# Kernel tuning notes

Hardware: AMD Instinct MI355X
Metric: run time of the kernel (lower is better)

The kernel has to match this reference:

```python
import jax, jax.numpy as jnp
import numpy as np

TEMPERATURE = 0.07
UNIFORMITY_THRESHOLD = 0.1
SEPARATION_MARGIN = 2.0
W_SUPCON = 1.0
W_SEPARATION = 0.5
W_UNIFORMITY = 0.5
NUM_MASKS = 6


def setup_inputs() -> dict:
    key = jax.random.key(0)
    k1, k2, k3 = jax.random.split(key, 3)
    B, H, Wd, D = 16, 33, 33, 512
    emb = jax.random.normal(k1, (B, H, Wd, D), dtype=jnp.float32)
    emb = emb / jnp.linalg.norm(emb, axis=-1, keepdims=True)  # module expects normalized embeddings
    masks = jax.random.uniform(k2, (B, NUM_MASKS, H, Wd), dtype=jnp.float32)
    is_forged = jax.random.uniform(k3, (B,), dtype=jnp.float32)
    return {"embeddings": emb, "masks": masks, "is_forged": is_forged}


def _labels(masks):
    # masks: (M, H, W). Channel i writes label i+1 where mask>0.5 (if channel has any mass);
    # later channels overwrite earlier -> equivalent to max over active hits.
    active = masks.sum(axis=(1, 2)) > 0  # (M,)
    hit = (masks > 0.5) & active[:, None, None]
    ids = jnp.arange(1, masks.shape[0] + 1)[:, None, None]
    return jnp.max(jnp.where(hit, ids, 0), axis=0).reshape(-1)  # (H*W,)


def _per_image(emb, masks, forged):
    H, W, D = emb.shape
    feat = emb.reshape(-1, D)  # (N, D)
    N = feat.shape[0]
    labels = _labels(masks)  # (N,) in 0..M
    L = masks.shape[0] + 1  # possible labels 0..6
    onehot = (labels[:, None] == jnp.arange(L)[None, :]).astype(feat.dtype)  # (N, L)
    cnt = onehot.sum(axis=0)  # (L,)
    sums = onehot.T @ feat  # (L, D) per-label sums
    mean_l = sums / jnp.maximum(cnt, 1.0)[:, None]  # safe per-label centroids

    # ---- SupCon (PixelSupConLoss) ----
    logits = (feat @ feat.T) / TEMPERATURE  # (N, N)
    logits = logits - jax.lax.stop_gradient(logits.max(axis=1, keepdims=True))
    same = (labels[:, None] == labels[None, :]).astype(feat.dtype)
    logits_mask = 1.0 - jnp.eye(N, dtype=feat.dtype)
    pos = same * logits_mask
    exp_l = jnp.exp(logits) * logits_mask
    log_prob = logits - jnp.log(exp_l.sum(axis=1, keepdims=True) + 1e-6)
    pos_sum = pos.sum(axis=1)
    mean_lp = (pos * log_prob).sum(axis=1) / jnp.where(pos_sum == 0, 1.0, pos_sum)
    anchor_valid = (pos_sum > 0).astype(feat.dtype)
    n_anchor = anchor_valid.sum()
    supcon = (-mean_lp * anchor_valid).sum() / jnp.maximum(n_anchor, 1.0)
    supcon_valid = n_anchor > 0

    # ---- Inter-instance separation ----
    present = cnt > 0
    cn = (mean_l ** 2).sum(axis=1)  # (L,)
    sq = cn[:, None] + cn[None, :] - 2.0 * (mean_l @ mean_l.T)  # squared centroid dists
    tri = jnp.triu(jnp.ones((L, L), dtype=bool), k=1)
    pair_valid = tri & present[:, None] & present[None, :]
    d = jnp.sqrt(jnp.where(pair_valid, jnp.maximum(sq, 0.0), 1.0))
    terms = jnp.where(pair_valid, jax.nn.relu(SEPARATION_MARGIN - d), 0.0)
    n_pairs = pair_valid.sum().astype(feat.dtype)
    sep = terms.sum() / jnp.maximum(n_pairs, 1.0)
    sep_valid = present.sum() >= 2

    # ---- Uniformity ----
    rn2 = (feat ** 2).sum(axis=1)  # (N,)
    q_l = onehot.T @ rn2  # (L,) per-label sum of squared norms
    var_l = q_l / jnp.maximum(cnt, 1.0) - (mean_l ** 2).sum(axis=1)  # E||e||^2 - ||mean||^2
    lbl_valid = (cnt >= 2) & (var_l > UNIFORMITY_THRESHOLD)
    inst_loss = jnp.where(lbl_valid, var_l - UNIFORMITY_THRESHOLD, 0.0).sum()
    n_lbl = lbl_valid.sum().astype(feat.dtype)
    uni_forged = inst_loss / jnp.maximum(n_lbl, 1.0)
    uni_forged_valid = n_lbl > 0
    mean_all = feat.mean(axis=0)
    var_all = ((feat - mean_all) ** 2).sum(axis=1).mean()
    uni_unf = jnp.where(var_all > UNIFORMITY_THRESHOLD, var_all - UNIFORMITY_THRESHOLD, 0.0)
    uni_unf_valid = var_all > UNIFORMITY_THRESHOLD

    is_f = forged >= 0.5
    uni = jnp.where(is_f, uni_forged, uni_unf)
    uni_valid = jnp.where(is_f, uni_forged_valid, uni_unf_valid)
    return supcon, supcon_valid, sep, sep_valid, uni, uni_valid


def _agg(vals, valids):
    v = valids.astype(vals.dtype)
    n = v.sum()
    return jnp.where(n > 0, (vals * v).sum() / jnp.maximum(n, 1.0), 0.0)


def reference(embeddings, masks, is_forged):
    sc, scv, sp, spv, un, unv = jax.vmap(_per_image)(embeddings, masks, is_forged)
    supcon = _agg(sc, scv)
    separation = _agg(sp, spv)
    uniformity = _agg(un, unv)
    return W_SUPCON * supcon + W_SEPARATION * separation + W_UNIFORMITY * uniformity
```

## Files before the change

kernel.cpp:

```cpp
#include <hip/hip_runtime.h>
#include <math.h>

#define NPIX 1089
#define DIM 512
#define NIMG 16
#define NLBL 8
#define NMASK 6
#define INVT 14.2857142857142857f

#define NGRP 72
#define NROWPAD 1152
#define NT9 9


typedef short v8s __attribute__((ext_vector_type(8)));
typedef float v4f __attribute__((ext_vector_type(4)));

__device__ __forceinline__ float wave_reduce(float x) {
#pragma unroll
  for (int o = 32; o > 0; o >>= 1) x += __shfl_xor(x, o, 64);
  return x;
}
__device__ __forceinline__ unsigned bfbits(float x) {
  unsigned u = __float_as_uint(x);
  return (u + 0x7FFFu + ((u >> 16) & 1u)) >> 16;
}
__device__ __forceinline__ unsigned pk(float lo, float hi) {
  return bfbits(lo) | (bfbits(hi) << 16);
}

__global__ __launch_bounds__(512) void k_packsum(const float* __restrict__ emb,
                                                 const float* __restrict__ masks,
                                                 uint2* __restrict__ bfemb2,
                                                 float* __restrict__ sums9,
                                                 int* __restrict__ labels,
                                                 float* __restrict__ cnt9,
                                                 unsigned* __restrict__ counter) {
  int b = blockIdx.y;
  int g9 = blockIdx.x >> 1, dh = blockIdx.x & 1;
  int tid = threadIdx.x, dd = tid & 63, w4 = tid >> 6, lane = tid & 63;
  __shared__ float msum[NMASK];
  __shared__ int slab[128];
  __shared__ int scnt[NLBL];
  __shared__ float4 red[8 * 8 * 64];
  if (tid < NMASK) msum[tid] = 0.f;
  if (tid < NLBL) scnt[tid] = 0;
  if (b == 0 && blockIdx.x == 0 && tid == 0) *counter = 0u;
  __syncthreads();
  {
    float am[NMASK] = {0.f, 0.f, 0.f, 0.f, 0.f, 0.f};
    for (int p = tid; p < NPIX; p += 512) {
#pragma unroll
      for (int c = 0; c < NMASK; c++) am[c] += masks[((size_t)b * NMASK + c) * NPIX + p];
    }
#pragma unroll
    for (int c = 0; c < NMASK; c++) {
      float v = wave_reduce(am[c]);
      if (lane == 0) atomicAdd(&msum[c], v);
    }
  }
  __syncthreads();
  if (tid < 128) {
    int r = g9 * 128 + tid;
    int lab = 7;
    if (r < NPIX) {
      lab = 0;
#pragma unroll
      for (int c = 0; c < NMASK; c++) {
        float mv = masks[((size_t)b * NMASK + c) * NPIX + r];
        if (mv > 0.5f && msum[c] > 0.f) lab = c + 1;
      }
    }
    slab[tid] = lab;
    if (dh == 0) {
      labels[b * NROWPAD + r] = lab;
      if (r < NPIX) atomicAdd(&scnt[lab], 1);
    }
  }
  __syncthreads();
  if (dh == 0 && tid < NLBL) cnt9[((size_t)b * NT9 + g9) * NLBL + tid] = (float)scnt[tid];
  float4 fa0 = {0,0,0,0}, fa1 = {0,0,0,0}, fa2 = {0,0,0,0}, fa3 = {0,0,0,0};
  float4 fa4 = {0,0,0,0}, fa5 = {0,0,0,0}, fa6 = {0,0,0,0}, fa7 = {0,0,0,0};
  int kc = dh * 8 + (dd >> 3), q = (dd >> 1) & 3, half = dd & 1;
#pragma unroll
  for (int k = 0; k < 16; k++) {
    int r = g9 * 128 + w4 + k * 8;
    bool v = r < NPIX;
    int rc = v ? r : (NPIX - 1);
    float4 x = ((const float4*)(emb + (size_t)(b * NPIX + rc) * DIM))[dh * 64 + dd];
    if (!v) x = make_float4(0.f, 0.f, 0.f, 0.f);
    uint2 o = make_uint2(pk(x.x, x.y), pk(x.z, x.w));
    bfemb2[((((size_t)(b * NGRP + (r >> 4)) * 16 + kc) * 64) + q * 16 + (r & 15)) * 2 + half] = o;
    int lab = __builtin_amdgcn_readfirstlane(slab[r - g9 * 128]);
    switch (lab) {
      case 0: fa0.x += x.x; fa0.y += x.y; fa0.z += x.z; fa0.w += x.w; break;
      case 1: fa1.x += x.x; fa1.y += x.y; fa1.z += x.z; fa1.w += x.w; break;
      case 2: fa2.x += x.x; fa2.y += x.y; fa2.z += x.z; fa2.w += x.w; break;
      case 3: fa3.x += x.x; fa3.y += x.y; fa3.z += x.z; fa3.w += x.w; break;
      case 4: fa4.x += x.x; fa4.y += x.y; fa4.z += x.z; fa4.w += x.w; break;
      case 5: fa5.x += x.x; fa5.y += x.y; fa5.z += x.z; fa5.w += x.w; break;
      case 6: fa6.x += x.x; fa6.y += x.y; fa6.z += x.z; fa6.w += x.w; break;
      default: fa7.x += x.x; fa7.y += x.y; fa7.z += x.z; fa7.w += x.w; break;
    }
  }
  red[(0 * 8 + w4) * 64 + dd] = fa0; red[(1 * 8 + w4) * 64 + dd] = fa1;
  red[(2 * 8 + w4) * 64 + dd] = fa2; red[(3 * 8 + w4) * 64 + dd] = fa3;
  red[(4 * 8 + w4) * 64 + dd] = fa4; red[(5 * 8 + w4) * 64 + dd] = fa5;
  red[(6 * 8 + w4) * 64 + dd] = fa6; red[(7 * 8 + w4) * 64 + dd] = fa7;
  __syncthreads();
  int l = tid >> 6, d2 = tid & 63;
  float4 s = {0,0,0,0};
#pragma unroll
  for (int ww = 0; ww < 8; ww++) {
    float4 t = red[(l * 8 + ww) * 64 + d2];
    s.x += t.x; s.y += t.y; s.z += t.z; s.w += t.w;
  }
  *(float4*)&sums9[(((size_t)(b * NT9 + g9) * NLBL + l) * DIM) + dh * 256 + d2 * 4] = s;
}

__global__ __launch_bounds__(512) void k_epass5(const uint4* __restrict__ bfemb4,
                                                float* __restrict__ E9) {
  int n = blockIdx.x;
  int img = ((n & 7) << 1) | ((n >> 3) & 1);
  int t = n >> 4;
  int it = 0, rem = t;
  while (rem >= NT9 - it) { rem -= NT9 - it; it++; }
  int jt = it + rem;
  int i0 = it * 128, j0 = jt * 128;
  bool diag = (it == jt);
  int tid = threadIdx.x, lane = tid & 63, w = tid >> 6;
  int wm = w >> 2, wn = w & 3;
  int quad = lane >> 4, l15 = lane & 15;
  __shared__ float Ered[4][128];
  __shared__ float Ecol[2][128];

  size_t uA[4], uB[2];
#pragma unroll
  for (int f = 0; f < 4; f++)
    uA[f] = ((size_t)(img * NGRP + it * 8 + wm * 4 + f) * 16) * 64 + lane;
#pragma unroll
  for (int f = 0; f < 2; f++)
    uB[f] = ((size_t)(img * NGRP + jt * 8 + wn * 2 + f) * 16) * 64 + lane;

  v4f acc[4][2];
#pragma unroll
  for (int mf = 0; mf < 4; mf++)
#pragma unroll
    for (int nf = 0; nf < 2; nf++) acc[mf][nf] = (v4f){0.f, 0.f, 0.f, 0.f};

  v8s a0[4], b0[2], a1[4], b1[2];
#define LOADG(kc, AR, BR)                                               \
  {                                                                     \
    _Pragma("unroll") for (int f = 0; f < 4; f++)                       \
        AR[f] = *(const v8s*)(bfemb4 + uA[f] + (kc) * 64);              \
    _Pragma("unroll") for (int f = 0; f < 2; f++)                       \
        BR[f] = *(const v8s*)(bfemb4 + uB[f] + (kc) * 64);              \
  }
#define MFMAG(AR, BR)                                                   \
  {                                                                     \
    _Pragma("unroll") for (int mf = 0; mf < 4; mf++)                    \
        _Pragma("unroll") for (int nf = 0; nf < 2; nf++)                \
            acc[mf][nf] = __builtin_amdgcn_mfma_f32_16x16x32_bf16(      \
                AR[mf], BR[nf], acc[mf][nf], 0, 0, 0);                  \
  }

  LOADG(0, a0, b0);
#pragma unroll
  for (int kc = 0; kc < 16; kc += 2) {
    if (kc + 1 < 16) LOADG(kc + 1, a1, b1);
    MFMAG(a0, b0);
    if (kc + 2 < 16) LOADG(kc + 2, a0, b0);
    MFMAG(a1, b1);
  }
#undef LOADG
#undef MFMAG

  float scol[2] = {0.f, 0.f};
#pragma unroll
  for (int mf = 0; mf < 4; mf++) {
#pragma unroll
    for (int rr = 0; rr < 4; rr++) {
      int i = i0 + wm * 64 + mf * 16 + quad * 4 + rr;
      float srow = 0.f;
#pragma unroll
      for (int nf = 0; nf < 2; nf++) {
        int j = j0 + wn * 32 + nf * 16 + l15;
        float e = __expf((acc[mf][nf][rr] - 1.f) * INVT);
        bool ok = (j < NPIX) && (!diag || (i != j && i < NPIX));
        e = ok ? e : 0.f;
        srow += e;
        scol[nf] += e;
      }
      srow += __shfl_xor(srow, 1); srow += __shfl_xor(srow, 2);
      srow += __shfl_xor(srow, 4); srow += __shfl_xor(srow, 8);
      if (l15 == 0) Ered[wn][wm * 64 + mf * 16 + quad * 4 + rr] = srow;
    }
  }
  if (!diag) {
#pragma unroll
    for (int nf = 0; nf < 2; nf++) {
      float s = scol[nf];
      s += __shfl_xor(s, 16); s += __shfl_xor(s, 32);
      if (quad == 0) Ecol[wm][wn * 32 + nf * 16 + l15] = s;
    }
  }
  __syncthreads();
  if (tid < 128) {
    E9[((size_t)img * NT9 + jt) * NROWPAD + i0 + tid] =
        Ered[0][tid] + Ered[1][tid] + Ered[2][tid] + Ered[3][tid];
    if (!diag)
      E9[((size_t)img * NT9 + it) * NROWPAD + j0 + tid] = Ecol[0][tid] + Ecol[1][tid];
  }
}

__global__ __launch_bounds__(512) void k_imgfinal(const float* __restrict__ sums9,
                                                  const int* __restrict__ labels,
                                                  const float* __restrict__ cnt9,
                                                  const float* __restrict__ E9,
                                                  const float* __restrict__ is_forged,
                                                  unsigned* __restrict__ counter,
                                                  float* __restrict__ per_img,
                                                  float* __restrict__ out) {
  int b = blockIdx.x, tid = threadIdx.x;
  int wave = tid >> 6, lane = tid & 63;
  __shared__ float ssum[NLBL * DIM];
  __shared__ float sCnt[NLBL], sR[NLBL][NLBL];
  __shared__ float sLog, sNA;
  if (tid < NLBL) {
    float s = 0.f;
#pragma unroll
    for (int g = 0; g < NT9; g++) s += cnt9[((size_t)b * NT9 + g) * NLBL + tid];
    sCnt[tid] = s;
  }
  if (tid == 0) { sLog = 0.f; sNA = 0.f; }
  for (int o = tid; o < NLBL * DIM; o += 512) {
    float s = 0.f;
#pragma unroll
    for (int g = 0; g < NT9; g++) s += sums9[((size_t)(b * NT9 + g) * NLBL * DIM) + o];
    ssum[o] = s;
  }
  __syncthreads();
  float ll = 0.f, na = 0.f;
  for (int p = tid; p < NPIX; p += 512) {
    int lab = labels[b * NROWPAD + p];
    if (sCnt[lab] >= 1.5f) {
      float e = 0.f;
#pragma unroll
      for (int s = 0; s < NT9; s++) e += E9[((size_t)b * NT9 + s) * NROWPAD + p];
      ll += __logf(e + 1e-6f);
      na += 1.f;
    }
  }
  ll = wave_reduce(ll); na = wave_reduce(na);
  if (lane == 0) { atomicAdd(&sLog, ll); atomicAdd(&sNA, na); }
  for (int t = wave; t < 36; t += 8) {
    int a = 0, tt = t;
    while (tt >= NLBL - a) { tt -= NLBL - a; a++; }
    int bb = a + tt;
    float d0 = 0.f;
    for (int k = lane; k < DIM; k += 64) d0 += ssum[a * DIM + k] * ssum[bb * DIM + k];
    d0 = wave_reduce(d0);
    if (lane == 0) sR[a][bb] = d0;
  }
  __syncthreads();
  if (tid == 0) {
    float spos = 0.f;
    for (int l = 0; l < NLBL; l++) {
      float c = sCnt[l];
      if (c >= 1.5f) spos += (sR[l][l] - c) * INVT / (c - 1.f) - c * INVT;
    }
    float nA = sNA;
    float sc = nA > 0.f ? (sLog - spos) / nA : 0.f;
    float scv = nA > 0.f ? 1.f : 0.f;
    float inv[NLBL]; int present[NLBL]; int nPres = 0;
    for (int l = 0; l < NLBL; l++) {
      present[l] = sCnt[l] > 0.f;
      nPres += present[l];
      inv[l] = 1.f / fmaxf(sCnt[l], 1.f);
    }
    float sepsum = 0.f; int npairs = 0;
    for (int a = 0; a < NLBL; a++)
      for (int c = a + 1; c < NLBL; c++)
        if (present[a] && present[c]) {
          float sq_ = sR[a][a] * inv[a] * inv[a] + sR[c][c] * inv[c] * inv[c]
                    - 2.f * sR[a][c] * inv[a] * inv[c];
          float dd = sqrtf(fmaxf(sq_, 0.f));
          sepsum += fmaxf(2.f - dd, 0.f);
          npairs++;
        }
    float sep = npairs > 0 ? sepsum / (float)npairs : 0.f;
    float sepv = nPres >= 2 ? 1.f : 0.f;
    float inst = 0.f; int nlbl = 0;
    for (int l = 0; l < NLBL; l++) {
      float var = 1.f - sR[l][l] * inv[l] * inv[l];
      if (sCnt[l] >= 2.f && var > 0.1f) { inst += var - 0.1f; nlbl++; }
    }
    float unif = nlbl > 0 ? inst / (float)nlbl : 0.f;
    float unifv = nlbl > 0 ? 1.f : 0.f;
    float tot2 = 0.f;
    for (int a = 0; a < NLBL; a++) {
      tot2 += sR[a][a];
      for (int c = a + 1; c < NLBL; c++) tot2 += 2.f * sR[a][c];
    }
    float Nf = (float)NPIX;
    float var_all = 1.f - tot2 / (Nf * Nf);
    float uniu = var_all > 0.1f ? var_all - 0.1f : 0.f;
    float uniuv = var_all > 0.1f ? 1.f : 0.f;
    bool isf = is_forged[b] >= 0.5f;
    per_img[b * 6 + 0] = sc;
    per_img[b * 6 + 1] = scv;
    per_img[b * 6 + 2] = sep;
    per_img[b * 6 + 3] = sepv;
    per_img[b * 6 + 4] = isf ? unif : uniu;
    per_img[b * 6 + 5] = isf ? unifv : uniuv;
    __threadfence();
    unsigned tk = atomicAdd(counter, 1u);
    if (tk == NIMG - 1) {
      __threadfence();
      float accv[3] = {0.f, 0.f, 0.f}, accn[3] = {0.f, 0.f, 0.f};
      for (int bb = 0; bb < NIMG; bb++)
        for (int m = 0; m < 3; m++) {
          float v = per_img[bb * 6 + m * 2], val = per_img[bb * 6 + m * 2 + 1];
          accv[m] += v * val; accn[m] += val;
        }
      float scA = accn[0] > 0.f ? accv[0] / accn[0] : 0.f;
      float sepA = accn[1] > 0.f ? accv[1] / accn[1] : 0.f;
      float uniA = accn[2] > 0.f ? accv[2] / accn[2] : 0.f;
      out[0] = 1.0f * scA + 0.5f * sepA + 0.5f * uniA;
    }
  }
}

extern "C" void kernel_launch(void* const* d_in, const int* in_sizes, int n_in,
                              void* d_out, int out_size, void* d_ws, size_t ws_size,
                              hipStream_t stream) {
  const float* emb = (const float*)d_in[0];
  const float* masks = (const float*)d_in[1];
  const float* isf = (const float*)d_in[2];
  float* out = (float*)d_out;
  char* ws = (char*)d_ws;
  size_t off = 0;
  uint4* bfemb4 = (uint4*)(ws + off);
  off += (size_t)NIMG * NGRP * 16 * 64 * 16;
  float* E9 = (float*)(ws + off);     off += sizeof(float) * NIMG * NT9 * NROWPAD;
  float* sums9 = (float*)(ws + off);  off += sizeof(float) * NIMG * NT9 * NLBL * DIM;
  int* labels = (int*)(ws + off);     off += sizeof(int) * NIMG * NROWPAD;
  float* cnt9 = (float*)(ws + off);   off += sizeof(float) * NIMG * NT9 * NLBL;
  float* per_img = (float*)(ws + off); off += sizeof(float) * NIMG * 6;
  off = (off + 127) & ~(size_t)127;
  unsigned* counter = (unsigned*)(ws + off); off += 128;

  k_packsum<<<dim3(18, NIMG), 512, 0, stream>>>(emb, masks, (uint2*)bfemb4, sums9,
                                                labels, cnt9, counter);
  k_epass5<<<45 * NIMG, 512, 0, stream>>>(bfemb4, E9);
  k_imgfinal<<<NIMG, 512, 0, stream>>>(sums9, labels, cnt9, E9, isf, counter, per_img, out);
}
```

Measured before the change: 134.0 us.

## Stage Gram tiles through LDS via direct global-to-LDS loads with double buffering

The Gram-matrix tile kernel now cooperatively loads each k-chunk of the A and B row groups into a double-buffered LDS area using global_load_lds, one fragment per wave, and reuses the B buffer as A on diagonal tiles. Previously each wave fetched its fragments straight from global memory into registers, so every fragment was loaded several times by different waves. The aim is to cut redundant global and L2 traffic and register pressure. In exchange it adds a block-wide barrier per k-step and depends on the async LDS load being complete before the following barrier.

```diff
diff --git a/kernel.cpp b/kernel.cpp
--- a/kernel.cpp
+++ b/kernel.cpp
@@ -118,7 +118,7 @@
   *(float4*)&sums9[(((size_t)(b * NT9 + g9) * NLBL + l) * DIM) + dh * 256 + d2 * 4] = s;
 }
 
-__global__ __launch_bounds__(512) void k_epass5(const uint4* __restrict__ bfemb4,
+__global__ __launch_bounds__(512) void k_epass6(const uint4* __restrict__ bfemb4,
                                                 float* __restrict__ E9) {
   int n = blockIdx.x;
   int img = ((n & 7) << 1) | ((n >> 3) & 1);
@@ -131,16 +131,24 @@
   int tid = threadIdx.x, lane = tid & 63, w = tid >> 6;
   int wm = w >> 2, wn = w & 3;
   int quad = lane >> 4, l15 = lane & 15;
+  __shared__ uint4 st[2][2][8][64];
   __shared__ float Ered[4][128];
   __shared__ float Ecol[2][128];
 
-  size_t uA[4], uB[2];
-#pragma unroll
-  for (int f = 0; f < 4; f++)
-    uA[f] = ((size_t)(img * NGRP + it * 8 + wm * 4 + f) * 16) * 64 + lane;
-#pragma unroll
-  for (int f = 0; f < 2; f++)
-    uB[f] = ((size_t)(img * NGRP + jt * 8 + wn * 2 + f) * 16) * 64 + lane;
+  size_t gA = ((size_t)(img * NGRP + it * 8 + w) * 16) * 64 + lane;
+  size_t gB = ((size_t)(img * NGRP + jt * 8 + w) * 16) * 64 + lane;
+  int bsel = diag ? 0 : 1;
+
+#define STAGE(kc, buf)                                                          \
+  {                                                                             \
+    __builtin_amdgcn_global_load_lds(                                           \
+        (const __attribute__((address_space(1))) void*)(bfemb4 + gA + (kc) * 64), \
+        (__attribute__((address_space(3))) void*)&st[buf][0][w][0], 16, 0, 0);  \
+    if (!diag)                                                                  \
+      __builtin_amdgcn_global_load_lds(                                         \
+          (const __attribute__((address_space(1))) void*)(bfemb4 + gB + (kc) * 64), \
+          (__attribute__((address_space(3))) void*)&st[buf][1][w][0], 16, 0, 0); \
+  }
 
   v4f acc[4][2];
 #pragma unroll
@@ -148,32 +156,26 @@
 #pragma unroll
     for (int nf = 0; nf < 2; nf++) acc[mf][nf] = (v4f){0.f, 0.f, 0.f, 0.f};
 
-  v8s a0[4], b0[2], a1[4], b1[2];
-#define LOADG(kc, AR, BR)                                               \
-  {                                                                     \
-    _Pragma("unroll") for (int f = 0; f < 4; f++)                       \
-        AR[f] = *(const v8s*)(bfemb4 + uA[f] + (kc) * 64);              \
-    _Pragma("unroll") for (int f = 0; f < 2; f++)                       \
-        BR[f] = *(const v8s*)(bfemb4 + uB[f] + (kc) * 64);              \
-  }
-#define MFMAG(AR, BR)                                                   \
-  {                                                                     \
-    _Pragma("unroll") for (int mf = 0; mf < 4; mf++)                    \
-        _Pragma("unroll") for (int nf = 0; nf < 2; nf++)                \
-            acc[mf][nf] = __builtin_amdgcn_mfma_f32_16x16x32_bf16(      \
-                AR[mf], BR[nf], acc[mf][nf], 0, 0, 0);                  \
-  }
-
-  LOADG(0, a0, b0);
-#pragma unroll
-  for (int kc = 0; kc < 16; kc += 2) {
-    if (kc + 1 < 16) LOADG(kc + 1, a1, b1);
-    MFMAG(a0, b0);
-    if (kc + 2 < 16) LOADG(kc + 2, a0, b0);
-    MFMAG(a1, b1);
-  }
-#undef LOADG
-#undef MFMAG
+  STAGE(0, 0);
+  __syncthreads();
+#pragma unroll
+  for (int kc = 0; kc < 16; kc++) {
+    int cur = kc & 1;
+    if (kc < 15) STAGE(kc + 1, cur ^ 1);
+    v8s a[4], b[2];
+#pragma unroll
+    for (int f = 0; f < 4; f++) a[f] = *(const v8s*)&st[cur][0][wm * 4 + f][lane];
+#pragma unroll
+    for (int f = 0; f < 2; f++) b[f] = *(const v8s*)&st[cur][bsel][wn * 2 + f][lane];
+#pragma unroll
+    for (int mf = 0; mf < 4; mf++)
+#pragma unroll
+      for (int nf = 0; nf < 2; nf++)
+        acc[mf][nf] = __builtin_amdgcn_mfma_f32_16x16x32_bf16(a[mf], b[nf],
+                                                              acc[mf][nf], 0, 0, 0);
+    __syncthreads();
+  }
+#undef STAGE
 
   float scol[2] = {0.f, 0.f};
 #pragma unroll
@@ -352,6 +354,6 @@
 
   k_packsum<<<dim3(18, NIMG), 512, 0, stream>>>(emb, masks, (uint2*)bfemb4, sums9,
                                                 labels, cnt9, counter);
-  k_epass5<<<45 * NIMG, 512, 0, stream>>>(bfemb4, E9);
+  k_epass6<<<45 * NIMG, 512, 0, stream>>>(bfemb4, E9);
   k_imgfinal<<<NIMG, 512, 0, stream>>>(sums9, labels, cnt9, E9, isf, counter, per_img, out);
 }
```

After: 123.2 us. -8.0%, faster.
